# Performance work log

Hardware: AMD Instinct MI355X
Metric: run time of the kernel (lower is better)

## Reference

```python
import jax, jax.numpy as jnp
import numpy as np

S, N, H, E, L = 2048, 32, 512, 256, 2


def setup_inputs() -> dict:
    key = jax.random.key(0)
    ks = jax.random.split(key, 16)
    s = 0.05  # weight scale for stability
    return {
        "x": jax.random.randint(ks[0], (N,), 0, 10),
        "encoder_states": jax.random.normal(ks[1], (S, N, 2 * H), jnp.float32),
        "hidden": jax.random.normal(ks[2], (L, N, H), jnp.float32),
        "cell": jax.random.normal(ks[3], (L, N, H), jnp.float32),
        "W_energy": jax.random.normal(ks[4], (1, 3 * H), jnp.float32) * s,
        "b_energy": jnp.zeros((1,), jnp.float32),
        "emb_table": jax.random.normal(ks[5], (10, E), jnp.float32),
        "wih0": jax.random.normal(ks[6], (4 * H, 2 * H + E), jnp.float32) * s,
        "whh0": jax.random.normal(ks[7], (4 * H, H), jnp.float32) * s,
        "bih0": jnp.zeros((4 * H,), jnp.float32),
        "bhh0": jnp.zeros((4 * H,), jnp.float32),
        "wih1": jax.random.normal(ks[8], (4 * H, H), jnp.float32) * s,
        "whh1": jax.random.normal(ks[9], (4 * H, H), jnp.float32) * s,
        "bih1": jnp.zeros((4 * H,), jnp.float32),
        "bhh1": jnp.zeros((4 * H,), jnp.float32),
        "Wc": jax.random.normal(ks[10], (10, H), jnp.float32) * s,
        "bc": jnp.zeros((10,), jnp.float32),
    }


def _lstm_cell(x, h, c, wih, whh, bih, bhh):
    # PyTorch gate order: i, f, g, o
    gates = x @ wih.T + bih + h @ whh.T + bhh  # [N, 4H]
    i, f, g, o = jnp.split(gates, 4, axis=-1)
    c_new = jax.nn.sigmoid(f) * c + jax.nn.sigmoid(i) * jnp.tanh(g)
    h_new = jax.nn.sigmoid(o) * jnp.tanh(c_new)
    return h_new, c_new


def reference(x, encoder_states, hidden, cell, W_energy, b_energy, emb_table,
              wih0, whh0, bih0, bhh0, wih1, whh1, bih1, bhh1, Wc, bc):
    seq_len = encoder_states.shape[0]
    h_last = hidden[-1]  # [N, H]
    h_rep = jnp.broadcast_to(h_last, (seq_len,) + h_last.shape)  # [S, N, H]
    cat = jnp.concatenate([h_rep, encoder_states], axis=2)  # [S, N, 3H]
    energy = jax.nn.relu(cat @ W_energy.T + b_energy)  # [S, N, 1]
    attn = jax.nn.softmax(energy, axis=0)  # softmax over seq dim
    context = jnp.einsum('snk,snl->knl', attn, encoder_states)  # [1, N, 2H]
    emb = emb_table[x][None]  # [1, N, E]
    inp = jnp.concatenate([context, emb], axis=2)[0]  # [N, 2H+E]
    h0, c0 = _lstm_cell(inp, hidden[0], cell[0], wih0, whh0, bih0, bhh0)
    h1, c1 = _lstm_cell(h0, hidden[1], cell[1], wih1, whh1, bih1, bhh1)
    predictions = h1 @ Wc.T + bc  # [N, 10]
    hidden_new = jnp.stack([h0, h1], axis=0)
    cell_new = jnp.stack([c0, c1], axis=0)
    return predictions, hidden_new, cell_new
```

## Files before the change

kernel.cpp:

```cpp
#include <hip/hip_runtime.h>

#define SS 2048
#define NN_ 32
#define HH 512
#define EE 256
#define TWO_H 1024

#define OUT_PRED 0
#define OUT_H0 320
#define OUT_H1 16704
#define OUT_C0 33088
#define OUT_C1 49472

#define WS_ACC 0
#define WS_SUMW 1048576
#define WS_XCAT0 1049600
#define WS_PG0 0
#define WS_XCAT1 458752
#define WS_PG1 491520

__device__ __forceinline__ float wave_reduce(float v) {
  v += __shfl_xor(v, 32);
  v += __shfl_xor(v, 16);
  v += __shfl_xor(v, 8);
  v += __shfl_xor(v, 4);
  v += __shfl_xor(v, 2);
  v += __shfl_xor(v, 1);
  return v;
}

__device__ __forceinline__ float sigmoidf_(float x) { return 1.0f / (1.0f + __expf(-x)); }

__global__ __launch_bounds__(256, 4) void attn_pass(
    const float* __restrict__ enc, const float* __restrict__ hidden,
    const float* __restrict__ We, const float* __restrict__ be,
    float* __restrict__ ws) {
  const int blk = blockIdx.x;
  const int n = blk >> 5;
  const int chunk = blk & 31;
  const int t = threadIdx.x;
  const int wave = t >> 6;
  const int lane = t & 63;

  const float* hl = hidden + (size_t)(NN_ + n) * HH;
  float cp;
  {
    float4 a = *(const float4*)(hl + lane * 8);
    float4 b = *(const float4*)(hl + lane * 8 + 4);
    float4 wa = *(const float4*)(We + lane * 8);
    float4 wb = *(const float4*)(We + lane * 8 + 4);
    cp = a.x * wa.x + a.y * wa.y + a.z * wa.z + a.w * wa.w +
         b.x * wb.x + b.y * wb.y + b.z * wb.z + b.w * wb.w;
  }
  cp = wave_reduce(cp);
  const float c_n = cp + be[0];

  const float4 w0 = *(const float4*)(We + HH + 0 * 256 + lane * 4);
  const float4 w1 = *(const float4*)(We + HH + 1 * 256 + lane * 4);
  const float4 w2 = *(const float4*)(We + HH + 2 * 256 + lane * 4);
  const float4 w3 = *(const float4*)(We + HH + 3 * 256 + lane * 4);

  float4 acc0 = {0, 0, 0, 0}, acc1 = {0, 0, 0, 0}, acc2 = {0, 0, 0, 0}, acc3 = {0, 0, 0, 0};
  float sumw = 0.f;

  const int sBase = chunk * 64 + wave * 16;
#pragma unroll 2
  for (int i = 0; i < 16; ++i) {
    const float* row = enc + ((size_t)(sBase + i) * NN_ + n) * TWO_H;
    float4 e0 = *(const float4*)(row + 0 * 256 + lane * 4);
    float4 e1 = *(const float4*)(row + 1 * 256 + lane * 4);
    float4 e2 = *(const float4*)(row + 2 * 256 + lane * 4);
    float4 e3 = *(const float4*)(row + 3 * 256 + lane * 4);
    float d = e0.x * w0.x + e0.y * w0.y + e0.z * w0.z + e0.w * w0.w +
              e1.x * w1.x + e1.y * w1.y + e1.z * w1.z + e1.w * w1.w +
              e2.x * w2.x + e2.y * w2.y + e2.z * w2.z + e2.w * w2.w +
              e3.x * w3.x + e3.y * w3.y + e3.z * w3.z + e3.w * w3.w;
    d = wave_reduce(d);
    float en = c_n + d;
    en = en > 0.f ? en : 0.f;
    float p = __expf(en - 4.0f);
    sumw += p;
    acc0.x = fmaf(p, e0.x, acc0.x); acc0.y = fmaf(p, e0.y, acc0.y);
    acc0.z = fmaf(p, e0.z, acc0.z); acc0.w = fmaf(p, e0.w, acc0.w);
    acc1.x = fmaf(p, e1.x, acc1.x); acc1.y = fmaf(p, e1.y, acc1.y);
    acc1.z = fmaf(p, e1.z, acc1.z); acc1.w = fmaf(p, e1.w, acc1.w);
    acc2.x = fmaf(p, e2.x, acc2.x); acc2.y = fmaf(p, e2.y, acc2.y);
    acc2.z = fmaf(p, e2.z, acc2.z); acc2.w = fmaf(p, e2.w, acc2.w);
    acc3.x = fmaf(p, e3.x, acc3.x); acc3.y = fmaf(p, e3.y, acc3.y);
    acc3.z = fmaf(p, e3.z, acc3.z); acc3.w = fmaf(p, e3.w, acc3.w);
  }

  __shared__ __align__(16) float lacc[4][1024];
  __shared__ float lsum[4];
  *(float4*)&lacc[wave][0 * 256 + lane * 4] = acc0;
  *(float4*)&lacc[wave][1 * 256 + lane * 4] = acc1;
  *(float4*)&lacc[wave][2 * 256 + lane * 4] = acc2;
  *(float4*)&lacc[wave][3 * 256 + lane * 4] = acc3;
  if (lane == 0) lsum[wave] = sumw;
  __syncthreads();

  const int j = t * 4;
  float4 o;
  o.x = lacc[0][j + 0] + lacc[1][j + 0] + lacc[2][j + 0] + lacc[3][j + 0];
  o.y = lacc[0][j + 1] + lacc[1][j + 1] + lacc[2][j + 1] + lacc[3][j + 1];
  o.z = lacc[0][j + 2] + lacc[1][j + 2] + lacc[2][j + 2] + lacc[3][j + 2];
  o.w = lacc[0][j + 3] + lacc[1][j + 3] + lacc[2][j + 3] + lacc[3][j + 3];
  *(float4*)&ws[WS_ACC + (size_t)blk * 1024 + j] = o;
  if (t == 0) ws[WS_SUMW + blk] = lsum[0] + lsum[1] + lsum[2] + lsum[3];
}

__global__ __launch_bounds__(256) void reduce_ctx(
    const int* __restrict__ x, const float* __restrict__ emb,
    const float* __restrict__ hidden, float* __restrict__ ws) {
  const int b = blockIdx.x;
  const int n = b >> 3;
  const int jg = b & 7;
  const int t = threadIdx.x;
  if (t < 128) {
    const int j = jg * 128 + t;
    float sumw = 0.f;
#pragma unroll
    for (int c = 0; c < 32; ++c) sumw += ws[WS_SUMW + n * 32 + c];
    const float inv = 1.0f / sumw;
    float v = 0.f;
#pragma unroll 8
    for (int c = 0; c < 32; ++c) v += ws[WS_ACC + (size_t)(n * 32 + c) * 1024 + j];
    ws[WS_XCAT0 + j * NN_ + n] = v * inv;
  } else if (t < 224) {
    const int row = jg * 96 + (t - 128);
    float v;
    if (row < 256) {
      v = emb[(size_t)x[n] * EE + row];
    } else {
      v = hidden[(size_t)n * HH + (row - 256)];
    }
    ws[WS_XCAT0 + (1024 + row) * NN_ + n] = v;
  }
}

__global__ __launch_bounds__(256, 2) void gates0_kernel(
    const float* __restrict__ wih0, const float* __restrict__ whh0, float* __restrict__ ws) {
  __shared__ __align__(16) float xs[256 * 32];
  __shared__ __align__(16) float wt[32 * 260];
  const int bid = blockIdx.x;
  const int chunk = bid % 7;
  const int hg = bid / 7;
  const int t = threadIdx.x;
  const int nn = t & 31;
  const int rl = t >> 5;

  {
    const float* src = ws + WS_XCAT0 + (size_t)chunk * 256 * 32;
#pragma unroll
    for (int i = t * 4; i < 8192; i += 1024)
      *(float4*)&xs[i] = *(const float4*)&src[i];
  }
  {
    const int r = t >> 3;
    const int k8 = t & 7;
    const int grow = (r >> 3) * 512 + hg * 8 + (r & 7);
    const float* src = (chunk < 5) ? (wih0 + (size_t)grow * 1280 + chunk * 256)
                                   : (whh0 + (size_t)grow * 512 + (chunk - 5) * 256);
#pragma unroll
    for (int jj = 0; jj < 8; ++jj) {
      const int kl = jj * 32 + k8 * 4;
      *(float4*)&wt[r * 260 + kl] = *(const float4*)(src + kl);
    }
  }
  __syncthreads();

  const float* w0p = &wt[(0 * 8 + rl) * 260];
  const float* w1p = &wt[(1 * 8 + rl) * 260];
  const float* w2p = &wt[(2 * 8 + rl) * 260];
  const float* w3p = &wt[(3 * 8 + rl) * 260];

  float a0 = 0.f, a1 = 0.f, a2 = 0.f, a3 = 0.f;
#pragma unroll 4
  for (int k = 0; k < 256; k += 4) {
    const float4 w0 = *(const float4*)(w0p + k);
    const float4 w1 = *(const float4*)(w1p + k);
    const float4 w2 = *(const float4*)(w2p + k);
    const float4 w3 = *(const float4*)(w3p + k);
    const float x0 = xs[(k + 0) * 32 + nn];
    const float x1 = xs[(k + 1) * 32 + nn];
    const float x2 = xs[(k + 2) * 32 + nn];
    const float x3 = xs[(k + 3) * 32 + nn];
    a0 += w0.x * x0 + w0.y * x1 + w0.z * x2 + w0.w * x3;
    a1 += w1.x * x0 + w1.y * x1 + w1.z * x2 + w1.w * x3;
    a2 += w2.x * x0 + w2.y * x1 + w2.z * x2 + w2.w * x3;
    a3 += w3.x * x0 + w3.y * x1 + w3.z * x2 + w3.w * x3;
  }

  const int h = hg * 8 + rl;
  float* dst = ws + WS_PG0 + ((size_t)chunk * 2048 + h) * 32 + nn;
  dst[0 * 512 * 32] = a0;
  dst[1 * 512 * 32] = a1;
  dst[2 * 512 * 32] = a2;
  dst[3 * 512 * 32] = a3;
}

__global__ __launch_bounds__(256) void lstm0_kernel(
    const float* __restrict__ cell, const float* __restrict__ hidden,
    const float* __restrict__ bih0, const float* __restrict__ bhh0,
    float* __restrict__ out, float* __restrict__ ws) {
  const int g = blockIdx.x * 256 + threadIdx.x;
  const int nn = g & 31;
  const int h = g >> 5;
  float gi = bih0[h] + bhh0[h];
  float gf = bih0[512 + h] + bhh0[512 + h];
  float gg = bih0[1024 + h] + bhh0[1024 + h];
  float go = bih0[1536 + h] + bhh0[1536 + h];
#pragma unroll
  for (int c = 0; c < 7; ++c) {
    const float* p = ws + WS_PG0 + (size_t)c * 2048 * 32;
    gi += p[(0 * 512 + h) * 32 + nn];
    gf += p[(1 * 512 + h) * 32 + nn];
    gg += p[(2 * 512 + h) * 32 + nn];
    go += p[(3 * 512 + h) * 32 + nn];
  }
  const float cprev = cell[(size_t)nn * HH + h];
  const float c0 = sigmoidf_(gf) * cprev + sigmoidf_(gi) * tanhf(gg);
  const float h0 = sigmoidf_(go) * tanhf(c0);
  out[OUT_H0 + nn * HH + h] = h0;
  out[OUT_C0 + nn * HH + h] = c0;
  ws[WS_XCAT1 + h * 32 + nn] = h0;
  ws[WS_XCAT1 + (512 + h) * 32 + nn] = hidden[(size_t)(NN_ + nn) * HH + h];
}

__global__ __launch_bounds__(256, 2) void gates1_kernel(
    const float* __restrict__ wih1, const float* __restrict__ whh1, float* __restrict__ ws) {
  __shared__ __align__(16) float xs[128 * 32];
  __shared__ __align__(16) float wt[32 * 132];
  const int bid = blockIdx.x;
  const int chunk = bid & 7;
  const int hg = bid >> 3;
  const int t = threadIdx.x;
  const int nn = t & 31;
  const int rl = t >> 5;
  const int kb = chunk * 128;

  {
    const float* src = ws + WS_XCAT1 + (size_t)kb * 32;
#pragma unroll
    for (int i = t * 4; i < 4096; i += 1024)
      *(float4*)&xs[i] = *(const float4*)&src[i];
  }
  {
    const int r = t >> 3;
    const int k8 = t & 7;
    const int grow = (r >> 3) * 512 + hg * 8 + (r & 7);
    const float* src = (chunk < 4) ? (wih1 + (size_t)grow * 512 + kb)
                                   : (whh1 + (size_t)grow * 512 + (kb - 512));
#pragma unroll
    for (int jj = 0; jj < 4; ++jj) {
      const int kl = jj * 32 + k8 * 4;
      *(float4*)&wt[r * 132 + kl] = *(const float4*)(src + kl);
    }
  }
  __syncthreads();

  const float* w0p = &wt[(0 * 8 + rl) * 132];
  const float* w1p = &wt[(1 * 8 + rl) * 132];
  const float* w2p = &wt[(2 * 8 + rl) * 132];
  const float* w3p = &wt[(3 * 8 + rl) * 132];

  float a0 = 0.f, a1 = 0.f, a2 = 0.f, a3 = 0.f;
#pragma unroll 4
  for (int k = 0; k < 128; k += 4) {
    const float4 w0 = *(const float4*)(w0p + k);
    const float4 w1 = *(const float4*)(w1p + k);
    const float4 w2 = *(const float4*)(w2p + k);
    const float4 w3 = *(const float4*)(w3p + k);
    const float x0 = xs[(k + 0) * 32 + nn];
    const float x1 = xs[(k + 1) * 32 + nn];
    const float x2 = xs[(k + 2) * 32 + nn];
    const float x3 = xs[(k + 3) * 32 + nn];
    a0 += w0.x * x0 + w0.y * x1 + w0.z * x2 + w0.w * x3;
    a1 += w1.x * x0 + w1.y * x1 + w1.z * x2 + w1.w * x3;
    a2 += w2.x * x0 + w2.y * x1 + w2.z * x2 + w2.w * x3;
    a3 += w3.x * x0 + w3.y * x1 + w3.z * x2 + w3.w * x3;
  }

  const int h = hg * 8 + rl;
  float* dst = ws + WS_PG1 + ((size_t)chunk * 2048 + h) * 32 + nn;
  dst[0 * 512 * 32] = a0;
  dst[1 * 512 * 32] = a1;
  dst[2 * 512 * 32] = a2;
  dst[3 * 512 * 32] = a3;
}

__global__ __launch_bounds__(256) void lstm1_kernel(
    const float* __restrict__ cell,
    const float* __restrict__ bih1, const float* __restrict__ bhh1,
    float* __restrict__ out, float* __restrict__ ws) {
  const int g = blockIdx.x * 256 + threadIdx.x;
  const int nn = g & 31;
  const int h = g >> 5;
  float gi = bih1[h] + bhh1[h];
  float gf = bih1[512 + h] + bhh1[512 + h];
  float gg = bih1[1024 + h] + bhh1[1024 + h];
  float go = bih1[1536 + h] + bhh1[1536 + h];
#pragma unroll
  for (int c = 0; c < 8; ++c) {
    const float* p = ws + WS_PG1 + (size_t)c * 2048 * 32;
    gi += p[(0 * 512 + h) * 32 + nn];
    gf += p[(1 * 512 + h) * 32 + nn];
    gg += p[(2 * 512 + h) * 32 + nn];
    go += p[(3 * 512 + h) * 32 + nn];
  }
  const float cprev = cell[(size_t)(NN_ + nn) * HH + h];
  const float c1 = sigmoidf_(gf) * cprev + sigmoidf_(gi) * tanhf(gg);
  const float h1 = sigmoidf_(go) * tanhf(c1);
  out[OUT_H1 + nn * HH + h] = h1;
  out[OUT_C1 + nn * HH + h] = c1;
}

__global__ __launch_bounds__(256) void pred_kernel(
    const float* __restrict__ Wc, const float* __restrict__ bc, float* out) {
  const int wid = blockIdx.x * 4 + (threadIdx.x >> 6);
  const int lane = threadIdx.x & 63;
  const int nn = wid / 10;
  const int c = wid % 10;
  const float* hp = out + OUT_H1 + (size_t)nn * HH;
  const float* wp = Wc + (size_t)c * HH;
  float p = 0.f;
#pragma unroll
  for (int j = 0; j < 8; ++j) p += hp[lane * 8 + j] * wp[lane * 8 + j];
  p = wave_reduce(p);
  if (lane == 0) out[OUT_PRED + nn * 10 + c] = p + bc[c];
}

extern "C" void kernel_launch(void* const* d_in, const int* in_sizes, int n_in,
                              void* d_out, int out_size, void* d_ws, size_t ws_size,
                              hipStream_t stream) {
  const int* x = (const int*)d_in[0];
  const float* enc = (const float*)d_in[1];
  const float* hidden = (const float*)d_in[2];
  const float* cell = (const float*)d_in[3];
  const float* We = (const float*)d_in[4];
  const float* be = (const float*)d_in[5];
  const float* emb = (const float*)d_in[6];
  const float* wih0 = (const float*)d_in[7];
  const float* whh0 = (const float*)d_in[8];
  const float* bih0 = (const float*)d_in[9];
  const float* bhh0 = (const float*)d_in[10];
  const float* wih1 = (const float*)d_in[11];
  const float* whh1 = (const float*)d_in[12];
  const float* bih1 = (const float*)d_in[13];
  const float* bhh1 = (const float*)d_in[14];
  const float* Wc = (const float*)d_in[15];
  const float* bc = (const float*)d_in[16];
  float* out = (float*)d_out;
  float* ws = (float*)d_ws;

  hipLaunchKernelGGL(attn_pass, dim3(1024), dim3(256), 0, stream, enc, hidden, We, be, ws);
  hipLaunchKernelGGL(reduce_ctx, dim3(256), dim3(256), 0, stream, x, emb, hidden, ws);
  hipLaunchKernelGGL(gates0_kernel, dim3(448), dim3(256), 0, stream, wih0, whh0, ws);
  hipLaunchKernelGGL(lstm0_kernel, dim3(64), dim3(256), 0, stream, cell, hidden, bih0, bhh0, out, ws);
  hipLaunchKernelGGL(gates1_kernel, dim3(512), dim3(256), 0, stream, wih1, whh1, ws);
  hipLaunchKernelGGL(lstm1_kernel, dim3(64), dim3(256), 0, stream, cell, bih1, bhh1, out, ws);
  hipLaunchKernelGGL(pred_kernel, dim3(80), dim3(256), 0, stream, Wc, bc, out);
}
```

Before: 78.94 us.

## Fuse context reduction and prediction into last-block tails, split gates0 finer

```diff
diff --git a/kernel.cpp b/kernel.cpp
--- a/kernel.cpp
+++ b/kernel.cpp
@@ -14,10 +14,11 @@
 
 #define WS_ACC 0
 #define WS_SUMW 1048576
-#define WS_XCAT0 1049600
+#define WS_CNT 1049600
+#define WS_XCAT0 1049664
 #define WS_PG0 0
-#define WS_XCAT1 458752
-#define WS_PG1 491520
+#define WS_XCAT1 1107008
+#define WS_PG1 1139776
 
 __device__ __forceinline__ float wave_reduce(float v) {
   v += __shfl_xor(v, 32);
@@ -34,6 +35,7 @@
 __global__ __launch_bounds__(256, 4) void attn_pass(
     const float* __restrict__ enc, const float* __restrict__ hidden,
     const float* __restrict__ We, const float* __restrict__ be,
+    const int* __restrict__ x, const float* __restrict__ emb,
     float* __restrict__ ws) {
   const int blk = blockIdx.x;
   const int n = blk >> 5;
@@ -92,6 +94,7 @@
 
   __shared__ __align__(16) float lacc[4][1024];
   __shared__ float lsum[4];
+  __shared__ int lastFlag;
   *(float4*)&lacc[wave][0 * 256 + lane * 4] = acc0;
   *(float4*)&lacc[wave][1 * 256 + lane * 4] = acc1;
   *(float4*)&lacc[wave][2 * 256 + lane * 4] = acc2;
@@ -107,150 +110,60 @@
   o.w = lacc[0][j + 3] + lacc[1][j + 3] + lacc[2][j + 3] + lacc[3][j + 3];
   *(float4*)&ws[WS_ACC + (size_t)blk * 1024 + j] = o;
   if (t == 0) ws[WS_SUMW + blk] = lsum[0] + lsum[1] + lsum[2] + lsum[3];
-}
-
-__global__ __launch_bounds__(256) void reduce_ctx(
-    const int* __restrict__ x, const float* __restrict__ emb,
-    const float* __restrict__ hidden, float* __restrict__ ws) {
-  const int b = blockIdx.x;
-  const int n = b >> 3;
-  const int jg = b & 7;
-  const int t = threadIdx.x;
-  if (t < 128) {
-    const int j = jg * 128 + t;
-    float sumw = 0.f;
-#pragma unroll
-    for (int c = 0; c < 32; ++c) sumw += ws[WS_SUMW + n * 32 + c];
-    const float inv = 1.0f / sumw;
+
+  __threadfence();
+  __syncthreads();
+  if (t == 0) {
+    int* cnt = (int*)(ws + WS_CNT);
+    lastFlag = (atomicAdd(&cnt[n], 1) == 31);
+  }
+  __syncthreads();
+  if (!lastFlag) return;
+  __threadfence();
+
+  float st = 0.f;
+#pragma unroll
+  for (int c = 0; c < 32; ++c) st += ws[WS_SUMW + n * 32 + c];
+  const float inv = 1.0f / st;
+#pragma unroll
+  for (int rep = 0; rep < 4; ++rep) {
+    const int jj = rep * 256 + t;
     float v = 0.f;
 #pragma unroll 8
-    for (int c = 0; c < 32; ++c) v += ws[WS_ACC + (size_t)(n * 32 + c) * 1024 + j];
-    ws[WS_XCAT0 + j * NN_ + n] = v * inv;
-  } else if (t < 224) {
-    const int row = jg * 96 + (t - 128);
-    float v;
-    if (row < 256) {
-      v = emb[(size_t)x[n] * EE + row];
-    } else {
-      v = hidden[(size_t)n * HH + (row - 256)];
-    }
-    ws[WS_XCAT0 + (1024 + row) * NN_ + n] = v;
-  }
-}
-
-__global__ __launch_bounds__(256, 2) void gates0_kernel(
+    for (int c = 0; c < 32; ++c) v += ws[WS_ACC + (size_t)(n * 32 + c) * 1024 + jj];
+    ws[WS_XCAT0 + jj * NN_ + n] = v * inv;
+  }
+  const int xi = x[n];
+  for (int i = t; i < 768; i += 256) {
+    float v = (i < 256) ? emb[(size_t)xi * EE + i]
+                        : hidden[(size_t)n * HH + (i - 256)];
+    ws[WS_XCAT0 + (1024 + i) * NN_ + n] = v;
+  }
+}
+
+__global__ __launch_bounds__(256, 4) void gates0_kernel(
     const float* __restrict__ wih0, const float* __restrict__ whh0, float* __restrict__ ws) {
-  __shared__ __align__(16) float xs[256 * 32];
-  __shared__ __align__(16) float wt[32 * 260];
+  __shared__ __align__(16) float xs[128 * 32];
+  __shared__ __align__(16) float wt[32 * 132];
   const int bid = blockIdx.x;
-  const int chunk = bid % 7;
-  const int hg = bid / 7;
+  const int chunk = bid % 14;
+  const int hg = bid / 14;
   const int t = threadIdx.x;
   const int nn = t & 31;
   const int rl = t >> 5;
 
   {
-    const float* src = ws + WS_XCAT0 + (size_t)chunk * 256 * 32;
-#pragma unroll
-    for (int i = t * 4; i < 8192; i += 1024)
+    const float* src = ws + WS_XCAT0 + (size_t)chunk * 128 * 32;
+#pragma unroll
+    for (int i = t * 4; i < 4096; i += 1024)
       *(float4*)&xs[i] = *(const float4*)&src[i];
   }
   {
     const int r = t >> 3;
     const int k8 = t & 7;
     const int grow = (r >> 3) * 512 + hg * 8 + (r & 7);
-    const float* src = (chunk < 5) ? (wih0 + (size_t)grow * 1280 + chunk * 256)
-                                   : (whh0 + (size_t)grow * 512 + (chunk - 5) * 256);
-#pragma unroll
-    for (int jj = 0; jj < 8; ++jj) {
-      const int kl = jj * 32 + k8 * 4;
-      *(float4*)&wt[r * 260 + kl] = *(const float4*)(src + kl);
-    }
-  }
-  __syncthreads();
-
-  const float* w0p = &wt[(0 * 8 + rl) * 260];
-  const float* w1p = &wt[(1 * 8 + rl) * 260];
-  const float* w2p = &wt[(2 * 8 + rl) * 260];
-  const float* w3p = &wt[(3 * 8 + rl) * 260];
-
-  float a0 = 0.f, a1 = 0.f, a2 = 0.f, a3 = 0.f;
-#pragma unroll 4
-  for (int k = 0; k < 256; k += 4) {
-    const float4 w0 = *(const float4*)(w0p + k);
-    const float4 w1 = *(const float4*)(w1p + k);
-    const float4 w2 = *(const float4*)(w2p + k);
-    const float4 w3 = *(const float4*)(w3p + k);
-    const float x0 = xs[(k + 0) * 32 + nn];
-    const float x1 = xs[(k + 1) * 32 + nn];
-    const float x2 = xs[(k + 2) * 32 + nn];
-    const float x3 = xs[(k + 3) * 32 + nn];
-    a0 += w0.x * x0 + w0.y * x1 + w0.z * x2 + w0.w * x3;
-    a1 += w1.x * x0 + w1.y * x1 + w1.z * x2 + w1.w * x3;
-    a2 += w2.x * x0 + w2.y * x1 + w2.z * x2 + w2.w * x3;
-    a3 += w3.x * x0 + w3.y * x1 + w3.z * x2 + w3.w * x3;
-  }
-
-  const int h = hg * 8 + rl;
-  float* dst = ws + WS_PG0 + ((size_t)chunk * 2048 + h) * 32 + nn;
-  dst[0 * 512 * 32] = a0;
-  dst[1 * 512 * 32] = a1;
-  dst[2 * 512 * 32] = a2;
-  dst[3 * 512 * 32] = a3;
-}
-
-__global__ __launch_bounds__(256) void lstm0_kernel(
-    const float* __restrict__ cell, const float* __restrict__ hidden,
-    const float* __restrict__ bih0, const float* __restrict__ bhh0,
-    float* __restrict__ out, float* __restrict__ ws) {
-  const int g = blockIdx.x * 256 + threadIdx.x;
-  const int nn = g & 31;
-  const int h = g >> 5;
-  float gi = bih0[h] + bhh0[h];
-  float gf = bih0[512 + h] + bhh0[512 + h];
-  float gg = bih0[1024 + h] + bhh0[1024 + h];
-  float go = bih0[1536 + h] + bhh0[1536 + h];
-#pragma unroll
-  for (int c = 0; c < 7; ++c) {
-    const float* p = ws + WS_PG0 + (size_t)c * 2048 * 32;
-    gi += p[(0 * 512 + h) * 32 + nn];
-    gf += p[(1 * 512 + h) * 32 + nn];
-    gg += p[(2 * 512 + h) * 32 + nn];
-    go += p[(3 * 512 + h) * 32 + nn];
-  }
-  const float cprev = cell[(size_t)nn * HH + h];
-  const float c0 = sigmoidf_(gf) * cprev + sigmoidf_(gi) * tanhf(gg);
-  const float h0 = sigmoidf_(go) * tanhf(c0);
-  out[OUT_H0 + nn * HH + h] = h0;
-  out[OUT_C0 + nn * HH + h] = c0;
-  ws[WS_XCAT1 + h * 32 + nn] = h0;
-  ws[WS_XCAT1 + (512 + h) * 32 + nn] = hidden[(size_t)(NN_ + nn) * HH + h];
-}
-
-__global__ __launch_bounds__(256, 2) void gates1_kernel(
-    const float* __restrict__ wih1, const float* __restrict__ whh1, float* __restrict__ ws) {
-  __shared__ __align__(16) float xs[128 * 32];
-  __shared__ __align__(16) float wt[32 * 132];
-  const int bid = blockIdx.x;
-  const int chunk = bid & 7;
-  const int hg = bid >> 3;
-  const int t = threadIdx.x;
-  const int nn = t & 31;
-  const int rl = t >> 5;
-  const int kb = chunk * 128;
-
-  {
-    const float* src = ws + WS_XCAT1 + (size_t)kb * 32;
-#pragma unroll
-    for (int i = t * 4; i < 4096; i += 1024)
-      *(float4*)&xs[i] = *(const float4*)&src[i];
-  }
-  {
-    const int r = t >> 3;
-    const int k8 = t & 7;
-    const int grow = (r >> 3) * 512 + hg * 8 + (r & 7);
-    const float* src = (chunk < 4) ? (wih1 + (size_t)grow * 512 + kb)
-                                   : (whh1 + (size_t)grow * 512 + (kb - 512));
+    const float* src = (chunk < 10) ? (wih0 + (size_t)grow * 1280 + chunk * 128)
+                                    : (whh0 + (size_t)grow * 512 + (chunk - 10) * 128);
 #pragma unroll
     for (int jj = 0; jj < 4; ++jj) {
       const int kl = jj * 32 + k8 * 4;
@@ -282,6 +195,96 @@
   }
 
   const int h = hg * 8 + rl;
+  float* dst = ws + WS_PG0 + ((size_t)chunk * 2048 + h) * 32 + nn;
+  dst[0 * 512 * 32] = a0;
+  dst[1 * 512 * 32] = a1;
+  dst[2 * 512 * 32] = a2;
+  dst[3 * 512 * 32] = a3;
+}
+
+__global__ __launch_bounds__(256) void lstm0_kernel(
+    const float* __restrict__ cell, const float* __restrict__ hidden,
+    const float* __restrict__ bih0, const float* __restrict__ bhh0,
+    float* __restrict__ out, float* __restrict__ ws) {
+  const int g = blockIdx.x * 256 + threadIdx.x;
+  const int nn = g & 31;
+  const int h = g >> 5;
+  float gi = bih0[h] + bhh0[h];
+  float gf = bih0[512 + h] + bhh0[512 + h];
+  float gg = bih0[1024 + h] + bhh0[1024 + h];
+  float go = bih0[1536 + h] + bhh0[1536 + h];
+#pragma unroll
+  for (int c = 0; c < 14; ++c) {
+    const float* p = ws + WS_PG0 + (size_t)c * 2048 * 32;
+    gi += p[(0 * 512 + h) * 32 + nn];
+    gf += p[(1 * 512 + h) * 32 + nn];
+    gg += p[(2 * 512 + h) * 32 + nn];
+    go += p[(3 * 512 + h) * 32 + nn];
+  }
+  const float cprev = cell[(size_t)nn * HH + h];
+  const float c0 = sigmoidf_(gf) * cprev + sigmoidf_(gi) * tanhf(gg);
+  const float h0 = sigmoidf_(go) * tanhf(c0);
+  out[OUT_H0 + nn * HH + h] = h0;
+  out[OUT_C0 + nn * HH + h] = c0;
+  ws[WS_XCAT1 + h * 32 + nn] = h0;
+  ws[WS_XCAT1 + (512 + h) * 32 + nn] = hidden[(size_t)(NN_ + nn) * HH + h];
+}
+
+__global__ __launch_bounds__(256, 2) void gates1_kernel(
+    const float* __restrict__ wih1, const float* __restrict__ whh1, float* __restrict__ ws) {
+  __shared__ __align__(16) float xs[128 * 32];
+  __shared__ __align__(16) float wt[32 * 132];
+  const int bid = blockIdx.x;
+  const int chunk = bid & 7;
+  const int hg = bid >> 3;
+  const int t = threadIdx.x;
+  const int nn = t & 31;
+  const int rl = t >> 5;
+  const int kb = chunk * 128;
+
+  {
+    const float* src = ws + WS_XCAT1 + (size_t)kb * 32;
+#pragma unroll
+    for (int i = t * 4; i < 4096; i += 1024)
+      *(float4*)&xs[i] = *(const float4*)&src[i];
+  }
+  {
+    const int r = t >> 3;
+    const int k8 = t & 7;
+    const int grow = (r >> 3) * 512 + hg * 8 + (r & 7);
+    const float* src = (chunk < 4) ? (wih1 + (size_t)grow * 512 + kb)
+                                   : (whh1 + (size_t)grow * 512 + (kb - 512));
+#pragma unroll
+    for (int jj = 0; jj < 4; ++jj) {
+      const int kl = jj * 32 + k8 * 4;
+      *(float4*)&wt[r * 132 + kl] = *(const float4*)(src + kl);
+    }
+  }
+  __syncthreads();
+
+  const float* w0p = &wt[(0 * 8 + rl) * 132];
+  const float* w1p = &wt[(1 * 8 + rl) * 132];
+  const float* w2p = &wt[(2 * 8 + rl) * 132];
+  const float* w3p = &wt[(3 * 8 + rl) * 132];
+
+  float a0 = 0.f, a1 = 0.f, a2 = 0.f, a3 = 0.f;
+#pragma unroll 4
+  for (int k = 0; k < 128; k += 4) {
+    const float4 w0 = *(const float4*)(w0p + k);
+    const float4 w1 = *(const float4*)(w1p + k);
+    const float4 w2 = *(const float4*)(w2p + k);
+    const float4 w3 = *(const float4*)(w3p + k);
+    const float x0 = xs[(k + 0) * 32 + nn];
+    const float x1 = xs[(k + 1) * 32 + nn];
+    const float x2 = xs[(k + 2) * 32 + nn];
+    const float x3 = xs[(k + 3) * 32 + nn];
+    a0 += w0.x * x0 + w0.y * x1 + w0.z * x2 + w0.w * x3;
+    a1 += w1.x * x0 + w1.y * x1 + w1.z * x2 + w1.w * x3;
+    a2 += w2.x * x0 + w2.y * x1 + w2.z * x2 + w2.w * x3;
+    a3 += w3.x * x0 + w3.y * x1 + w3.z * x2 + w3.w * x3;
+  }
+
+  const int h = hg * 8 + rl;
   float* dst = ws + WS_PG1 + ((size_t)chunk * 2048 + h) * 32 + nn;
   dst[0 * 512 * 32] = a0;
   dst[1 * 512 * 32] = a1;
@@ -292,8 +295,10 @@
 __global__ __launch_bounds__(256) void lstm1_kernel(
     const float* __restrict__ cell,
     const float* __restrict__ bih1, const float* __restrict__ bhh1,
+    const float* __restrict__ Wc, const float* __restrict__ bc,
     float* __restrict__ out, float* __restrict__ ws) {
-  const int g = blockIdx.x * 256 + threadIdx.x;
+  const int t = threadIdx.x;
+  const int g = blockIdx.x * 256 + t;
   const int nn = g & 31;
   const int h = g >> 5;
   float gi = bih1[h] + bhh1[h];
@@ -313,21 +318,34 @@
   const float h1 = sigmoidf_(go) * tanhf(c1);
   out[OUT_H1 + nn * HH + h] = h1;
   out[OUT_C1 + nn * HH + h] = c1;
-}
-
-__global__ __launch_bounds__(256) void pred_kernel(
-    const float* __restrict__ Wc, const float* __restrict__ bc, float* out) {
-  const int wid = blockIdx.x * 4 + (threadIdx.x >> 6);
-  const int lane = threadIdx.x & 63;
-  const int nn = wid / 10;
-  const int c = wid % 10;
-  const float* hp = out + OUT_H1 + (size_t)nn * HH;
-  const float* wp = Wc + (size_t)c * HH;
-  float p = 0.f;
-#pragma unroll
-  for (int j = 0; j < 8; ++j) p += hp[lane * 8 + j] * wp[lane * 8 + j];
-  p = wave_reduce(p);
-  if (lane == 0) out[OUT_PRED + nn * 10 + c] = p + bc[c];
+
+  __shared__ int lastFlag;
+  __threadfence();
+  __syncthreads();
+  if (t == 0) {
+    int* cnt = (int*)(ws + WS_CNT);
+    lastFlag = (atomicAdd(&cnt[32], 1) == 63);
+  }
+  __syncthreads();
+  if (!lastFlag) return;
+  __threadfence();
+
+  const int wid = t >> 6;
+  const int lane = t & 63;
+  for (int o = wid; o < 320; o += 4) {
+    const int on = o / 10;
+    const int oc = o % 10;
+    const float* hp = out + OUT_H1 + (size_t)on * HH;
+    const float* wp = Wc + (size_t)oc * HH;
+    float4 ha = *(const float4*)(hp + lane * 8);
+    float4 hb = *(const float4*)(hp + lane * 8 + 4);
+    float4 wa = *(const float4*)(wp + lane * 8);
+    float4 wb = *(const float4*)(wp + lane * 8 + 4);
+    float p = ha.x * wa.x + ha.y * wa.y + ha.z * wa.z + ha.w * wa.w +
+              hb.x * wb.x + hb.y * wb.y + hb.z * wb.z + hb.w * wb.w;
+    p = wave_reduce(p);
+    if (lane == 0) out[OUT_PRED + on * 10 + oc] = p + bc[oc];
+  }
 }
 
 extern "C" void kernel_launch(void* const* d_in, const int* in_sizes, int n_in,
@@ -353,11 +371,11 @@
   float* out = (float*)d_out;
   float* ws = (float*)d_ws;
 
-  hipLaunchKernelGGL(attn_pass, dim3(1024), dim3(256), 0, stream, enc, hidden, We, be, ws);
-  hipLaunchKernelGGL(reduce_ctx, dim3(256), dim3(256), 0, stream, x, emb, hidden, ws);
-  hipLaunchKernelGGL(gates0_kernel, dim3(448), dim3(256), 0, stream, wih0, whh0, ws);
+  hipMemsetAsync((char*)d_ws + (size_t)WS_CNT * sizeof(float), 0, 256, stream);
+
+  hipLaunchKernelGGL(attn_pass, dim3(1024), dim3(256), 0, stream, enc, hidden, We, be, x, emb, ws);
+  hipLaunchKernelGGL(gates0_kernel, dim3(896), dim3(256), 0, stream, wih0, whh0, ws);
   hipLaunchKernelGGL(lstm0_kernel, dim3(64), dim3(256), 0, stream, cell, hidden, bih0, bhh0, out, ws);
   hipLaunchKernelGGL(gates1_kernel, dim3(512), dim3(256), 0, stream, wih1, whh1, ws);
-  hipLaunchKernelGGL(lstm1_kernel, dim3(64), dim3(256), 0, stream, cell, bih1, bhh1, out, ws);
-  hipLaunchKernelGGL(pred_kernel, dim3(80), dim3(256), 0, stream, Wc, bc, out);
-}
+  hipLaunchKernelGGL(lstm1_kernel, dim3(64), dim3(256), 0, stream, cell, bih1, bhh1, Wc, bc, out, ws);
+}
```

Result: slower. 272.6 us (+245.3%).

## Batch attention row loads, interleave wave reductions, and reorder block mapping

Applied to the files above, without the earlier changes.

```diff
diff --git a/kernel.cpp b/kernel.cpp
--- a/kernel.cpp
+++ b/kernel.cpp
@@ -16,8 +16,8 @@
 #define WS_SUMW 1048576
 #define WS_XCAT0 1049600
 #define WS_PG0 0
-#define WS_XCAT1 458752
-#define WS_PG1 491520
+#define WS_XCAT1 1107008
+#define WS_PG1 1139776
 
 __device__ __forceinline__ float wave_reduce(float v) {
   v += __shfl_xor(v, 32);
@@ -36,8 +36,8 @@
     const float* __restrict__ We, const float* __restrict__ be,
     float* __restrict__ ws) {
   const int blk = blockIdx.x;
-  const int n = blk >> 5;
-  const int chunk = blk & 31;
+  const int chunk = blk >> 5;
+  const int n = blk & 31;
   const int t = threadIdx.x;
   const int wave = t >> 6;
   const int lane = t & 63;
@@ -64,30 +64,50 @@
   float sumw = 0.f;
 
   const int sBase = chunk * 64 + wave * 16;
-#pragma unroll 2
-  for (int i = 0; i < 16; ++i) {
-    const float* row = enc + ((size_t)(sBase + i) * NN_ + n) * TWO_H;
-    float4 e0 = *(const float4*)(row + 0 * 256 + lane * 4);
-    float4 e1 = *(const float4*)(row + 1 * 256 + lane * 4);
-    float4 e2 = *(const float4*)(row + 2 * 256 + lane * 4);
-    float4 e3 = *(const float4*)(row + 3 * 256 + lane * 4);
-    float d = e0.x * w0.x + e0.y * w0.y + e0.z * w0.z + e0.w * w0.w +
-              e1.x * w1.x + e1.y * w1.y + e1.z * w1.z + e1.w * w1.w +
-              e2.x * w2.x + e2.y * w2.y + e2.z * w2.z + e2.w * w2.w +
-              e3.x * w3.x + e3.y * w3.y + e3.z * w3.z + e3.w * w3.w;
-    d = wave_reduce(d);
-    float en = c_n + d;
-    en = en > 0.f ? en : 0.f;
-    float p = __expf(en - 4.0f);
-    sumw += p;
-    acc0.x = fmaf(p, e0.x, acc0.x); acc0.y = fmaf(p, e0.y, acc0.y);
-    acc0.z = fmaf(p, e0.z, acc0.z); acc0.w = fmaf(p, e0.w, acc0.w);
-    acc1.x = fmaf(p, e1.x, acc1.x); acc1.y = fmaf(p, e1.y, acc1.y);
-    acc1.z = fmaf(p, e1.z, acc1.z); acc1.w = fmaf(p, e1.w, acc1.w);
-    acc2.x = fmaf(p, e2.x, acc2.x); acc2.y = fmaf(p, e2.y, acc2.y);
-    acc2.z = fmaf(p, e2.z, acc2.z); acc2.w = fmaf(p, e2.w, acc2.w);
-    acc3.x = fmaf(p, e3.x, acc3.x); acc3.y = fmaf(p, e3.y, acc3.y);
-    acc3.z = fmaf(p, e3.z, acc3.z); acc3.w = fmaf(p, e3.w, acc3.w);
+  const float* base = enc + ((size_t)sBase * NN_ + n) * TWO_H + lane * 4;
+
+#pragma unroll 1
+  for (int b = 0; b < 4; ++b) {
+    float4 e[4][4];
+#pragma unroll
+    for (int i = 0; i < 4; ++i) {
+      const float* row = base + (size_t)(b * 4 + i) * (NN_ * TWO_H);
+#pragma unroll
+      for (int q = 0; q < 4; ++q) e[i][q] = *(const float4*)(row + q * 256);
+    }
+    float d[4];
+#pragma unroll
+    for (int i = 0; i < 4; ++i) {
+      float s0 = e[i][0].x * w0.x + e[i][0].y * w0.y + e[i][0].z * w0.z + e[i][0].w * w0.w;
+      float s1 = e[i][1].x * w1.x + e[i][1].y * w1.y + e[i][1].z * w1.z + e[i][1].w * w1.w;
+      float s2 = e[i][2].x * w2.x + e[i][2].y * w2.y + e[i][2].z * w2.z + e[i][2].w * w2.w;
+      float s3 = e[i][3].x * w3.x + e[i][3].y * w3.y + e[i][3].z * w3.z + e[i][3].w * w3.w;
+      d[i] = (s0 + s1) + (s2 + s3);
+    }
+#pragma unroll
+    for (int m = 32; m >= 1; m >>= 1) {
+#pragma unroll
+      for (int i = 0; i < 4; ++i) d[i] += __shfl_xor(d[i], m);
+    }
+    float p[4];
+#pragma unroll
+    for (int i = 0; i < 4; ++i) {
+      float en = c_n + d[i];
+      en = en > 0.f ? en : 0.f;
+      p[i] = __expf(en - 4.0f);
+      sumw += p[i];
+    }
+#pragma unroll
+    for (int i = 0; i < 4; ++i) {
+      acc0.x = fmaf(p[i], e[i][0].x, acc0.x); acc0.y = fmaf(p[i], e[i][0].y, acc0.y);
+      acc0.z = fmaf(p[i], e[i][0].z, acc0.z); acc0.w = fmaf(p[i], e[i][0].w, acc0.w);
+      acc1.x = fmaf(p[i], e[i][1].x, acc1.x); acc1.y = fmaf(p[i], e[i][1].y, acc1.y);
+      acc1.z = fmaf(p[i], e[i][1].z, acc1.z); acc1.w = fmaf(p[i], e[i][1].w, acc1.w);
+      acc2.x = fmaf(p[i], e[i][2].x, acc2.x); acc2.y = fmaf(p[i], e[i][2].y, acc2.y);
+      acc2.z = fmaf(p[i], e[i][2].z, acc2.z); acc2.w = fmaf(p[i], e[i][2].w, acc2.w);
+      acc3.x = fmaf(p[i], e[i][3].x, acc3.x); acc3.y = fmaf(p[i], e[i][3].y, acc3.y);
+      acc3.z = fmaf(p[i], e[i][3].z, acc3.z); acc3.w = fmaf(p[i], e[i][3].w, acc3.w);
+    }
   }
 
   __shared__ __align__(16) float lacc[4][1024];
@@ -120,11 +140,11 @@
     const int j = jg * 128 + t;
     float sumw = 0.f;
 #pragma unroll
-    for (int c = 0; c < 32; ++c) sumw += ws[WS_SUMW + n * 32 + c];
+    for (int c = 0; c < 32; ++c) sumw += ws[WS_SUMW + c * 32 + n];
     const float inv = 1.0f / sumw;
     float v = 0.f;
 #pragma unroll 8
-    for (int c = 0; c < 32; ++c) v += ws[WS_ACC + (size_t)(n * 32 + c) * 1024 + j];
+    for (int c = 0; c < 32; ++c) v += ws[WS_ACC + (size_t)(c * 32 + n) * 1024 + j];
     ws[WS_XCAT0 + j * NN_ + n] = v * inv;
   } else if (t < 224) {
     const int row = jg * 96 + (t - 128);
```

New measurement: 84.08 us. +6.5%, slower.
